# Kernel optimization log

Hardware: AMD Instinct MI355X
Metric: run time of the kernel (lower is better)

## Reference

```python
import jax, jax.numpy as jnp
import numpy as np

B, DIM, HID = 16384, 512, 256
DT, N_STEPS = 0.1, 3


def setup_inputs() -> dict:
    key = jax.random.key(0)
    ks = jax.random.split(key, 5)
    z = jax.random.normal(ks[0], (B, DIM), dtype=jnp.float32)
    # HNN energy MLP: 2*DIM -> HID -> HID -> 1 (tanh activations)
    s1 = 1.0 / np.sqrt(2 * DIM)
    s2 = 1.0 / np.sqrt(HID)
    W1 = jax.random.normal(ks[1], (2 * DIM, HID), dtype=jnp.float32) * s1
    b1 = jnp.zeros((HID,), dtype=jnp.float32)
    W2 = jax.random.normal(ks[2], (HID, HID), dtype=jnp.float32) * s2
    b2 = jnp.zeros((HID,), dtype=jnp.float32)
    W3 = jax.random.normal(ks[3], (HID, 1), dtype=jnp.float32) * s2
    b3 = jnp.zeros((1,), dtype=jnp.float32)
    return {"z": z, "W1": W1, "b1": b1, "W2": W2, "b2": b2, "W3": W3, "b3": b3}


def reference(z, W1, b1, W2, b2, W3, b3):
    d = z.shape[-1]
    dt = jnp.float32(DT)

    def H_sum(zp):  # total Hamiltonian over the batch -> scalar
        h = jnp.tanh(zp @ W1 + b1)
        h = jnp.tanh(h @ W2 + b2)
        return jnp.sum(h @ W3 + b3)

    gradH = jax.grad(H_sum)  # [B, 2d]: (dH/dq, dH/dp) per sample

    def leapfrog(zp):
        q, p = zp[:, :d], zp[:, d:]
        # half-step momentum: dp/dt = -dH/dq
        g = gradH(jnp.concatenate([q, p], axis=-1))
        p = p - 0.5 * dt * g[:, :d]
        # full-step position: dq/dt = dH/dp
        g = gradH(jnp.concatenate([q, p], axis=-1))
        q = q + dt * g[:, d:]
        # half-step momentum
        g = gradH(jnp.concatenate([q, p], axis=-1))
        p = p - 0.5 * dt * g[:, :d]
        return jnp.concatenate([q, p], axis=-1)

    zp = jnp.concatenate([z, jnp.zeros_like(z)], axis=-1)  # phase space [B, 2d]
    for _ in range(N_STEPS):  # fixed small unroll (n_steps=3)
        zp = leapfrog(zp)
    return zp[:, :d]
```

## Files before the change

### kernel.cpp

```cpp
#include <hip/hip_runtime.h>
#include <math.h>

#define DT 0.1f

typedef __attribute__((ext_vector_type(4)))  short short4v;
typedef __attribute__((ext_vector_type(8)))  short short8;
typedef __attribute__((ext_vector_type(16))) float f32x16;

__device__ __forceinline__ short f2bf(float x) {
    unsigned int u = __float_as_uint(x);
    unsigned int r = (u + 0x7fffu + ((u >> 16) & 1u)) >> 16;
    return (short)r;
}
__device__ __forceinline__ float bf2f(short s) {
    return __uint_as_float(((unsigned int)(unsigned short)s) << 16);
}
__device__ __forceinline__ float tanh_fast(float x) {
    float e = __expf(x + x);
    float r = __builtin_amdgcn_rcpf(e + 1.f);
    return __builtin_fmaf(-2.f, r, 1.f);
}

__device__ __forceinline__ void pack32_body(const float* __restrict__ W,
                                            short* __restrict__ out,
                                            int K, int N, int idx, bool trans)
{
    int j = idx & 7, lane = (idx >> 3) & 63, rest = idx >> 9;
    int KT = K >> 4;
    int kt = rest % KT, nt = rest / KT;
    int k = kt * 16 + (lane >> 5) * 8 + j;
    int n = nt * 32 + (lane & 31);
    out[idx] = f2bf(trans ? W[n * K + k] : W[k * N + n]);
}

__global__ __launch_bounds__(256)
void prep(const float* __restrict__ W1, const float* __restrict__ W2,
          const float* __restrict__ z,
          short* __restrict__ PBSq, short* __restrict__ PBSp,
          short* __restrict__ PB2, short* __restrict__ PB2T,
          short* __restrict__ PB1q, short* __restrict__ PB1Tp,
          short* __restrict__ zpA)
{
    __shared__ short zb[32 * 520];
    const int tid = threadIdx.x;
    const int b = blockIdx.x;

    if (b < 512) {
        const int n = tid;
        float s[8];
#pragma unroll
        for (int i = 0; i < 8; ++i) s[i] = 0.f;
        int k; float coef; short* dst;
        if (b < 256) {
            k = b; coef = -0.5f * DT; dst = PBSq;
            for (int c = 0; c < 512; c += 8) {
#pragma unroll
                for (int i = 0; i < 8; ++i)
                    s[i] = __builtin_fmaf(W1[(c + i) * 256 + k],
                                          W1[(512 + c + i) * 256 + n], s[i]);
            }
        } else {
            k = b - 256; coef = DT; dst = PBSp;
            for (int c = 0; c < 512; c += 8) {
#pragma unroll
                for (int i = 0; i < 8; ++i)
                    s[i] = __builtin_fmaf(W1[(512 + c + i) * 256 + k],
                                          W1[(c + i) * 256 + n], s[i]);
            }
        }
        float v = coef * (((s[0] + s[1]) + (s[2] + s[3])) +
                          ((s[4] + s[5]) + (s[6] + s[7])));
        int kt = k >> 4, r = k & 15;
        int lane = (r >> 3) * 32 + (n & 31), nt = n >> 5;
        dst[(((nt * 16 + kt) * 64 + lane) << 3) + (r & 7)] = f2bf(v);
    } else if (b < 768) {
        pack32_body(W2, PB2, 256, 256, (b - 512) * 256 + tid, false);
    } else if (b < 1024) {
        pack32_body(W2, PB2T, 256, 256, (b - 768) * 256 + tid, true);
    } else if (b < 1536) {
        pack32_body(W1, PB1q, 512, 256, (b - 1024) * 256 + tid, false);
    } else if (b < 2048) {
        pack32_body(W1 + 512 * 256, PB1Tp, 256, 512, (b - 1536) * 256 + tid, true);
    } else {
        const int bx = b - 2048;
#pragma unroll
        for (int j = 0; j < 16; ++j) {
            int lin = j * 256 + tid;
            int r = lin >> 7, c4 = lin & 127;
            float4 v = ((const float4*)z)[(size_t)(bx * 32 + r) * 128 + c4];
            short4v pk;
            pk.x = f2bf(v.x); pk.y = f2bf(v.y); pk.z = f2bf(v.z); pk.w = f2bf(v.w);
            *(short4v*)&zb[r * 520 + c4 * 4] = pk;
        }
        __syncthreads();
        const int lane = tid & 63, w = tid >> 6;
        const int m = lane & 31, lh = lane >> 5;
#pragma unroll
        for (int j = 0; j < 8; ++j) {
            int kt = w * 8 + j;
            short8 f = *(const short8*)&zb[m * 520 + kt * 16 + lh * 8];
            *(short8*)(zpA + (((size_t)bx * 32 + kt) * 64 + lane) * 8) = f;
        }
    }
}

__device__ __forceinline__ short8 lds_frag(const short* Ac, int kt, int mt2,
                                           int l31, int lh, int rot)
{
    int nt_s = kt >> 1;
    int po = (((kt & 1) * 2 + lh) * 4 + rot) & 15;
    int base = ((nt_s * 2 + mt2) * 64 + l31) * 16 + po;
    short4v x = *(const short4v*)&Ac[base];
    short4v y = *(const short4v*)&Ac[base + 512];
    short8 r;
    r[0] = x.x; r[1] = x.y; r[2] = x.z; r[3] = x.w;
    r[4] = y.x; r[5] = y.y; r[6] = y.z; r[7] = y.w;
    return r;
}
__device__ __forceinline__ void store_tile(short* Ac, int nt, int mt2, int lane,
                                           int rot, const f32x16 v)
{
    int base = ((nt * 2 + mt2) * 64 + lane) * 16;
#pragma unroll
    for (int c = 0; c < 4; ++c) {
        short4v pk;
        pk.x = f2bf(v[4 * c + 0]); pk.y = f2bf(v[4 * c + 1]);
        pk.z = f2bf(v[4 * c + 2]); pk.w = f2bf(v[4 * c + 3]);
        *(short4v*)&Ac[base + ((4 * c + rot) & 15)] = pk;
    }
}

__device__ __forceinline__ void preload8(const short8* __restrict__ Bf, short8* pb)
{
#pragma unroll
    for (int k = 0; k < 8; ++k) pb[k] = Bf[k * 64];
}

__device__ __forceinline__ void gemm_nt(const short* Ac, int l31, int lh, int rot,
                                        const short8* __restrict__ Bf,
                                        short8* pb, f32x16& acc0, f32x16& acc1)
{
    short8 pa0[2], pa1[2];
    pa0[0] = lds_frag(Ac, 0, 0, l31, lh, rot);
    pa1[0] = lds_frag(Ac, 0, 1, l31, lh, rot);
    pa0[1] = lds_frag(Ac, 1, 0, l31, lh, rot);
    pa1[1] = lds_frag(Ac, 1, 1, l31, lh, rot);
#pragma unroll
    for (int kt = 0; kt < 16; ++kt) {
        short8 ca0 = pa0[kt & 1], ca1 = pa1[kt & 1], cb = pb[kt & 7];
        if (kt + 8 < 16) pb[kt & 7] = Bf[(kt + 8) * 64];
        if (kt + 2 < 16) {
            pa0[kt & 1] = lds_frag(Ac, kt + 2, 0, l31, lh, rot);
            pa1[kt & 1] = lds_frag(Ac, kt + 2, 1, l31, lh, rot);
        }
        acc0 = __builtin_amdgcn_mfma_f32_32x32x16_bf16(ca0, cb, acc0, 0, 0, 0);
        acc1 = __builtin_amdgcn_mfma_f32_32x32x16_bf16(ca1, cb, acc1, 0, 0, 0);
    }
}

__global__ __launch_bounds__(512, 1)
void mega(const short* __restrict__ zpA,
          const short* __restrict__ PB1q,
          const short* __restrict__ PB2,
          const short* __restrict__ PB2T,
          const short* __restrict__ PBSq,
          const short* __restrict__ PBSp,
          const float* __restrict__ b1,
          const float* __restrict__ b2,
          const float* __restrict__ W3,
          const short* __restrict__ PB1Tp,
          const float* __restrict__ z,
          float* __restrict__ out)
{
    __shared__ alignas(16) short smem[49152];
    short* h1_c = smem;
    short* da2_c = smem + 16384;
    short* da1_c = smem + 32768;

    const int tid = threadIdx.x;
    const int lane = tid & 63, w = tid >> 6;
    const int l31 = lane & 31, lh = lane >> 5;
    const int rot = ((l31 >> 2) & 3) * 4;
    const int bx = blockIdx.x;

    const int col = w * 32 + l31;
    const float b1v = b1[col], b2v = b2[col], w3v = W3[col];

    const short8* BfPB2  = (const short8*)PB2  + ((size_t)w * 16) * 64 + lane;
    const short8* BfPB2T = (const short8*)PB2T + ((size_t)w * 16) * 64 + lane;
    const short8* BfSq   = (const short8*)PBSq + ((size_t)w * 16) * 64 + lane;
    const short8* BfSp   = (const short8*)PBSp + ((size_t)w * 16) * 64 + lane;

    f32x16 A1[2];  A1[0] = 0.f; A1[1] = 0.f;
    f32x16 dsum[2]; dsum[0] = 0.f; dsum[1] = 0.f;
    short8 pb[8];

    {
        const short8* Af0 = (const short8*)zpA + ((size_t)(bx * 2 + 0) * 32) * 64 + lane;
        const short8* Af1 = (const short8*)zpA + ((size_t)(bx * 2 + 1) * 32) * 64 + lane;
        const short8* Bf  = (const short8*)PB1q + ((size_t)w * 32) * 64 + lane;
        short8 pa0[2], pa1[2];
#pragma unroll
        for (int k = 0; k < 2; ++k) { pa0[k] = Af0[k * 64]; pa1[k] = Af1[k * 64]; }
        preload8(Bf, pb);
#pragma unroll
        for (int kt = 0; kt < 32; ++kt) {
            short8 ca0 = pa0[kt & 1], ca1 = pa1[kt & 1], cb = pb[kt & 7];
            if (kt + 2 < 32) {
                pa0[kt & 1] = Af0[(kt + 2) * 64];
                pa1[kt & 1] = Af1[(kt + 2) * 64];
            }
            if (kt + 8 < 32) pb[kt & 7] = Bf[(kt + 8) * 64];
            A1[0] = __builtin_amdgcn_mfma_f32_32x32x16_bf16(ca0, cb, A1[0], 0, 0, 0);
            A1[1] = __builtin_amdgcn_mfma_f32_32x32x16_bf16(ca1, cb, A1[1], 0, 0, 0);
        }
    }

    preload8(BfPB2, pb);

    for (int it = 0; it < 8; ++it) {
        const bool isq = ((it % 3) == 1);

#pragma unroll
        for (int t = 0; t < 2; ++t) {
            f32x16 hv;
#pragma unroll
            for (int r = 0; r < 16; ++r) hv[r] = tanh_fast(A1[t][r] + b1v);
            store_tile(h1_c, w, t, lane, rot, hv);
        }
        __syncthreads();

        {
            f32x16 t0 = 0.f, t1 = 0.f;
            gemm_nt(h1_c, l31, lh, rot, BfPB2, pb, t0, t1);
            preload8(BfPB2T, pb);
#pragma unroll
            for (int t = 0; t < 2; ++t) {
                f32x16& tt = t ? t1 : t0;
                f32x16 d;
#pragma unroll
                for (int r = 0; r < 16; ++r) {
                    float ta = tanh_fast(tt[r] + b2v);
                    d[r] = w3v * (1.f - ta * ta);
                }
                store_tile(da2_c, w, t, lane, rot, d);
            }
        }
        __syncthreads();

        {
            f32x16 t0 = 0.f, t1 = 0.f;
            gemm_nt(da2_c, l31, lh, rot, BfPB2T, pb, t0, t1);
            if (it < 7) preload8(isq ? BfSp : BfSq, pb);
#pragma unroll
            for (int t = 0; t < 2; ++t) {
                f32x16& tt = t ? t1 : t0;
                f32x16 d;
                const int basei = ((w * 2 + t) * 64 + lane) * 16;
#pragma unroll
                for (int c = 0; c < 4; ++c) {
                    short4v h4 = *(const short4v*)&h1_c[basei + ((4 * c + rot) & 15)];
                    float h0 = bf2f(h4.x), h1f = bf2f(h4.y);
                    float h2 = bf2f(h4.z), h3 = bf2f(h4.w);
                    d[4 * c + 0] = tt[4 * c + 0] * (1.f - h0 * h0);
                    d[4 * c + 1] = tt[4 * c + 1] * (1.f - h1f * h1f);
                    d[4 * c + 2] = tt[4 * c + 2] * (1.f - h2 * h2);
                    d[4 * c + 3] = tt[4 * c + 3] * (1.f - h3 * h3);
                }
                if (isq) dsum[t] += d;
                store_tile(da1_c, w, t, lane, rot, d);
            }
        }
        __syncthreads();

        if (it < 7) {
            gemm_nt(da1_c, l31, lh, rot, isq ? BfSp : BfSq, pb, A1[0], A1[1]);
            preload8(BfPB2, pb);
        }
    }

    store_tile(h1_c, w, 0, lane, rot, dsum[0]);
    store_tile(h1_c, w, 1, lane, rot, dsum[1]);
    __syncthreads();

    const int mt2 = w >> 3 ? 0 : 0;
    const int mtg = w >> 2 & 1;
    (void)mt2; (void)mtg;

    f32x16 acc2[2];
    acc2[0] = 0.f; acc2[1] = 0.f;
    const int mt = w >> 2;
    const int nq = w & 3;
    {
        const short8* Bf0 = (const short8*)PB1Tp + (size_t)(nq * 4 + 0) * 16 * 64 + lane;
        const short8* Bf1 = (const short8*)PB1Tp + (size_t)(nq * 4 + 1) * 16 * 64 + lane;
        const short8* Bf2 = (const short8*)PB1Tp + (size_t)(nq * 4 + 2) * 16 * 64 + lane;
        const short8* Bf3 = (const short8*)PB1Tp + (size_t)(nq * 4 + 3) * 16 * 64 + lane;
        f32x16 acc4[4];
#pragma unroll
        for (int t = 0; t < 4; ++t) acc4[t] = 0.f;
        short8 br[2][4];
#pragma unroll
        for (int k = 0; k < 2; ++k) {
            br[k][0] = Bf0[k * 64]; br[k][1] = Bf1[k * 64];
            br[k][2] = Bf2[k * 64]; br[k][3] = Bf3[k * 64];
        }
#pragma unroll
        for (int kt = 0; kt < 16; ++kt) {
            short8 a = lds_frag(h1_c, kt, mt, l31, lh, rot);
            short8 bb[4];
#pragma unroll
            for (int t = 0; t < 4; ++t) bb[t] = br[kt & 1][t];
            if (kt + 2 < 16) {
                br[kt & 1][0] = Bf0[(kt + 2) * 64];
                br[kt & 1][1] = Bf1[(kt + 2) * 64];
                br[kt & 1][2] = Bf2[(kt + 2) * 64];
                br[kt & 1][3] = Bf3[(kt + 2) * 64];
            }
#pragma unroll
            for (int t = 0; t < 4; ++t)
                acc4[t] = __builtin_amdgcn_mfma_f32_32x32x16_bf16(a, bb[t], acc4[t], 0, 0, 0);
        }
        __syncthreads();

        float* Ct = (float*)smem;
#pragma unroll
        for (int p = 0; p < 2; ++p) {
            if (mt == p) {
#pragma unroll
                for (int t = 0; t < 4; ++t) {
                    const int c = (nq * 4 + t) * 32 + l31;
#pragma unroll
                    for (int r = 0; r < 16; ++r) {
                        int row = (r & 3) + 8 * (r >> 2) + 4 * lh;
                        Ct[row * 512 + c] = acc4[t][r];
                    }
                }
            }
            __syncthreads();
#pragma unroll
            for (int j = 0; j < 8; ++j) {
                int lin = j * 512 + tid;
                int r = lin >> 7, c4 = lin & 127;
                size_t gi = (size_t)(bx * 64 + p * 32 + r) * 128 + c4;
                float4 zv = ((const float4*)z)[gi];
                float4 cv = *(const float4*)&Ct[r * 512 + c4 * 4];
                float4 ov;
                ov.x = zv.x + DT * cv.x; ov.y = zv.y + DT * cv.y;
                ov.z = zv.z + DT * cv.z; ov.w = zv.w + DT * cv.w;
                ((float4*)out)[gi] = ov;
            }
            __syncthreads();
        }
    }
}

extern "C" void kernel_launch(void* const* d_in, const int* in_sizes, int n_in,
                              void* d_out, int out_size, void* d_ws, size_t ws_size,
                              hipStream_t stream)
{
    const float* z  = (const float*)d_in[0];
    const float* W1 = (const float*)d_in[1];
    const float* b1 = (const float*)d_in[2];
    const float* W2 = (const float*)d_in[3];
    const float* b2 = (const float*)d_in[4];
    const float* W3 = (const float*)d_in[5];
    float* out = (float*)d_out;

    short* PB2   = (short*)d_ws;
    short* PB2T  = PB2   + 65536;
    short* PBSq  = PB2T  + 65536;
    short* PBSp  = PBSq  + 65536;
    short* PB1q  = PBSp  + 65536;
    short* PB1Tp = PB1q  + 131072;
    short* zpA   = PB1Tp + 131072;

    prep<<<2560, 256, 0, stream>>>(W1, W2, z, PBSq, PBSp, PB2, PB2T,
                                   PB1q, PB1Tp, zpA);
    mega<<<256, 512, 0, stream>>>(zpA, PB1q, PB2, PB2T, PBSq, PBSp,
                                  b1, b2, W3, PB1Tp, z, out);
}
```

Baseline: 203.7 us.

## Use packed bf16 conversion and explicit vmcnt-gated B loads in gemm_nt

Replaces the manual round-to-nearest bf16 conversion with the hardware v_cvt_pk_bf16_f32 instruction when packing tiles and z. Restructures gemm_nt to issue its own 8 B-fragment global loads through inline asm, with per-iteration s_waitcnt vmcnt gating, and single-buffers the LDS A fragments. This drops the cross-stage preload of the next GEMM's weights that used to overlap with tanh epilogues. The first-layer GEMM's B prefetch depth shrinks from 8 to 4. The aim is fewer conversion ALU ops and lower register pressure, but global load latency is now exposed at the start of each GEMM.

```diff
diff --git a/kernel.cpp b/kernel.cpp
--- a/kernel.cpp
+++ b/kernel.cpp
@@ -19,6 +19,16 @@
     float e = __expf(x + x);
     float r = __builtin_amdgcn_rcpf(e + 1.f);
     return __builtin_fmaf(-2.f, r, 1.f);
+}
+__device__ __forceinline__ unsigned cvt_pk_bf16(float a, float b) {
+    unsigned r;
+    asm("v_cvt_pk_bf16_f32 %0, %1, %2" : "=v"(r) : "v"(a), "v"(b));
+    return r;
+}
+__device__ __forceinline__ short8 ldg8(const short8* p) {
+    short8 r;
+    asm volatile("global_load_dwordx4 %0, %1, off" : "=v"(r) : "v"(p));
+    return r;
 }
 
 __device__ __forceinline__ void pack32_body(const float* __restrict__ W,
@@ -88,9 +98,10 @@
             int lin = j * 256 + tid;
             int r = lin >> 7, c4 = lin & 127;
             float4 v = ((const float4*)z)[(size_t)(bx * 32 + r) * 128 + c4];
-            short4v pk;
-            pk.x = f2bf(v.x); pk.y = f2bf(v.y); pk.z = f2bf(v.z); pk.w = f2bf(v.w);
-            *(short4v*)&zb[r * 520 + c4 * 4] = pk;
+            uint2 pk;
+            pk.x = cvt_pk_bf16(v.x, v.y);
+            pk.y = cvt_pk_bf16(v.z, v.w);
+            *(uint2*)&zb[r * 520 + c4 * 4] = pk;
         }
         __syncthreads();
         const int lane = tid & 63, w = tid >> 6;
@@ -123,35 +134,33 @@
     int base = ((nt * 2 + mt2) * 64 + lane) * 16;
 #pragma unroll
     for (int c = 0; c < 4; ++c) {
-        short4v pk;
-        pk.x = f2bf(v[4 * c + 0]); pk.y = f2bf(v[4 * c + 1]);
-        pk.z = f2bf(v[4 * c + 2]); pk.w = f2bf(v[4 * c + 3]);
-        *(short4v*)&Ac[base + ((4 * c + rot) & 15)] = pk;
-    }
-}
-
-__device__ __forceinline__ void preload8(const short8* __restrict__ Bf, short8* pb)
-{
-#pragma unroll
-    for (int k = 0; k < 8; ++k) pb[k] = Bf[k * 64];
+        uint2 pk;
+        pk.x = cvt_pk_bf16(v[4 * c + 0], v[4 * c + 1]);
+        pk.y = cvt_pk_bf16(v[4 * c + 2], v[4 * c + 3]);
+        *(uint2*)&Ac[base + ((4 * c + rot) & 15)] = pk;
+    }
 }
 
 __device__ __forceinline__ void gemm_nt(const short* Ac, int l31, int lh, int rot,
                                         const short8* __restrict__ Bf,
-                                        short8* pb, f32x16& acc0, f32x16& acc1)
-{
-    short8 pa0[2], pa1[2];
-    pa0[0] = lds_frag(Ac, 0, 0, l31, lh, rot);
-    pa1[0] = lds_frag(Ac, 0, 1, l31, lh, rot);
-    pa0[1] = lds_frag(Ac, 1, 0, l31, lh, rot);
-    pa1[1] = lds_frag(Ac, 1, 1, l31, lh, rot);
+                                        f32x16& acc0, f32x16& acc1)
+{
+    asm volatile("s_waitcnt vmcnt(0)" ::: "memory");
+    short8 pb[8];
+#pragma unroll
+    for (int k = 0; k < 8; ++k) pb[k] = ldg8(Bf + k * 64);
+    short8 pa0 = lds_frag(Ac, 0, 0, l31, lh, rot);
+    short8 pa1 = lds_frag(Ac, 0, 1, l31, lh, rot);
 #pragma unroll
     for (int kt = 0; kt < 16; ++kt) {
-        short8 ca0 = pa0[kt & 1], ca1 = pa1[kt & 1], cb = pb[kt & 7];
-        if (kt + 8 < 16) pb[kt & 7] = Bf[(kt + 8) * 64];
-        if (kt + 2 < 16) {
-            pa0[kt & 1] = lds_frag(Ac, kt + 2, 0, l31, lh, rot);
-            pa1[kt & 1] = lds_frag(Ac, kt + 2, 1, l31, lh, rot);
+        const int N = (15 - kt) < 7 ? (15 - kt) : 7;
+        asm volatile("s_waitcnt vmcnt(%1)" : "+v"(pb[kt & 7]) : "i"(N));
+        short8 cb = pb[kt & 7];
+        if (kt + 8 < 16) pb[kt & 7] = ldg8(Bf + (kt + 8) * 64);
+        short8 ca0 = pa0, ca1 = pa1;
+        if (kt + 1 < 16) {
+            pa0 = lds_frag(Ac, kt + 1, 0, l31, lh, rot);
+            pa1 = lds_frag(Ac, kt + 1, 1, l31, lh, rot);
         }
         acc0 = __builtin_amdgcn_mfma_f32_32x32x16_bf16(ca0, cb, acc0, 0, 0, 0);
         acc1 = __builtin_amdgcn_mfma_f32_32x32x16_bf16(ca1, cb, acc1, 0, 0, 0);
@@ -193,31 +202,29 @@
 
     f32x16 A1[2];  A1[0] = 0.f; A1[1] = 0.f;
     f32x16 dsum[2]; dsum[0] = 0.f; dsum[1] = 0.f;
-    short8 pb[8];
 
     {
         const short8* Af0 = (const short8*)zpA + ((size_t)(bx * 2 + 0) * 32) * 64 + lane;
         const short8* Af1 = (const short8*)zpA + ((size_t)(bx * 2 + 1) * 32) * 64 + lane;
         const short8* Bf  = (const short8*)PB1q + ((size_t)w * 32) * 64 + lane;
-        short8 pa0[2], pa1[2];
+        short8 pa0[2], pa1[2], pb[4];
 #pragma unroll
         for (int k = 0; k < 2; ++k) { pa0[k] = Af0[k * 64]; pa1[k] = Af1[k * 64]; }
-        preload8(Bf, pb);
+#pragma unroll
+        for (int k = 0; k < 4; ++k) pb[k] = Bf[k * 64];
 #pragma unroll
         for (int kt = 0; kt < 32; ++kt) {
-            short8 ca0 = pa0[kt & 1], ca1 = pa1[kt & 1], cb = pb[kt & 7];
+            short8 ca0 = pa0[kt & 1], ca1 = pa1[kt & 1], cb = pb[kt & 3];
             if (kt + 2 < 32) {
                 pa0[kt & 1] = Af0[(kt + 2) * 64];
                 pa1[kt & 1] = Af1[(kt + 2) * 64];
             }
-            if (kt + 8 < 32) pb[kt & 7] = Bf[(kt + 8) * 64];
+            if (kt + 4 < 32) pb[kt & 3] = Bf[(kt + 4) * 64];
             A1[0] = __builtin_amdgcn_mfma_f32_32x32x16_bf16(ca0, cb, A1[0], 0, 0, 0);
             A1[1] = __builtin_amdgcn_mfma_f32_32x32x16_bf16(ca1, cb, A1[1], 0, 0, 0);
         }
     }
 
-    preload8(BfPB2, pb);
-
     for (int it = 0; it < 8; ++it) {
         const bool isq = ((it % 3) == 1);
 
@@ -232,8 +239,7 @@
 
         {
             f32x16 t0 = 0.f, t1 = 0.f;
-            gemm_nt(h1_c, l31, lh, rot, BfPB2, pb, t0, t1);
-            preload8(BfPB2T, pb);
+            gemm_nt(h1_c, l31, lh, rot, BfPB2, t0, t1);
 #pragma unroll
             for (int t = 0; t < 2; ++t) {
                 f32x16& tt = t ? t1 : t0;
@@ -250,8 +256,7 @@
 
         {
             f32x16 t0 = 0.f, t1 = 0.f;
-            gemm_nt(da2_c, l31, lh, rot, BfPB2T, pb, t0, t1);
-            if (it < 7) preload8(isq ? BfSp : BfSq, pb);
+            gemm_nt(da2_c, l31, lh, rot, BfPB2T, t0, t1);
 #pragma unroll
             for (int t = 0; t < 2; ++t) {
                 f32x16& tt = t ? t1 : t0;
@@ -274,8 +279,7 @@
         __syncthreads();
 
         if (it < 7) {
-            gemm_nt(da1_c, l31, lh, rot, isq ? BfSp : BfSq, pb, A1[0], A1[1]);
-            preload8(BfPB2, pb);
+            gemm_nt(da1_c, l31, lh, rot, isq ? BfSp : BfSq, A1[0], A1[1]);
         }
     }
 
@@ -283,12 +287,6 @@
     store_tile(h1_c, w, 1, lane, rot, dsum[1]);
     __syncthreads();
 
-    const int mt2 = w >> 3 ? 0 : 0;
-    const int mtg = w >> 2 & 1;
-    (void)mt2; (void)mtg;
-
-    f32x16 acc2[2];
-    acc2[0] = 0.f; acc2[1] = 0.f;
     const int mt = w >> 2;
     const int nq = w & 3;
     {
```

Measured after the change: 195.6 us. 4.0% less time.
